# Kernel tuning notes

Hardware: AMD Instinct MI355X
Metric: run time of the kernel (lower is better)

Reference implementation:

```python
import jax, jax.numpy as jnp
import numpy as np
import math

N_HEAD = 32
HEAD_DIM = 64
ROTARY_DIM = 32
ROTARY_BASE = 10000.0
NEG_INF = -10000.0


def _rope_cos_sin(seqlen):
    # RotaryEmbedding._update_cos_sin_cache: inv_freq over even indices of rotary_dim
    inv_freq = 1.0 / (ROTARY_BASE ** (jnp.arange(0, ROTARY_DIM, 2, dtype=jnp.float32) / ROTARY_DIM))
    t = jnp.arange(seqlen, dtype=jnp.float32)
    freqs = jnp.outer(t, inv_freq)  # [s, rd/2]
    return jnp.cos(freqs), jnp.sin(freqs)


def _apply_rotary(t, cos, sin):
    # t: [b, s, h, d]; GPT-NeoX half-rotation on first ROTARY_DIM dims, pass-through rest
    half = ROTARY_DIM // 2
    x1 = t[..., :half]
    x2 = t[..., half:ROTARY_DIM]
    x_pass = t[..., ROTARY_DIM:]
    c = cos[:, None, :]  # [s, 1, rd/2] -> broadcasts over (b, s, h, rd/2)
    s_ = sin[:, None, :]
    return jnp.concatenate([x1 * c - x2 * s_, x1 * s_ + x2 * c, x_pass], axis=-1)


def setup_inputs() -> dict:
    key = jax.random.key(0)
    k1, k2, k3, k4, k5 = jax.random.split(key, 5)
    b, s, e = 2, 2048, 2048
    return {
        "x": jax.random.normal(k1, (b, s, e), dtype=jnp.float32),
        "Wqkv": jax.random.normal(k2, (e, 3 * e), dtype=jnp.float32) * 0.02,
        "bqkv": jax.random.normal(k3, (3 * e,), dtype=jnp.float32) * 0.02,
        "Wout": jax.random.normal(k4, (e, e), dtype=jnp.float32) * 0.02,
        "bout": jax.random.normal(k5, (e,), dtype=jnp.float32) * 0.02,
    }


def reference(x, Wqkv, bqkv, Wout, bout):
    b, s, e = x.shape
    # QKV projection -> [b, s, 3, h, d]
    qkv = (x @ Wqkv + bqkv).reshape(b, s, 3, N_HEAD, HEAD_DIM)
    cos, sin = _rope_cos_sin(s)
    q = _apply_rotary(qkv[:, :, 0], cos, sin)
    k = _apply_rotary(qkv[:, :, 1], cos, sin)
    v = qkv[:, :, 2]
    # Attention (SelfAttention/CrossAttention math, fp32, materialized scores)
    scale = 1.0 / math.sqrt(HEAD_DIM)
    scores = jnp.einsum('bthd,bshd->bhts', q, k * scale)  # [b, h, s, s]
    rows = jnp.arange(s)[:, None]
    cols = jnp.arange(s)[None, :]
    causal_mask = cols > rows  # seqlen_q == seqlen_k
    scores = jnp.where(causal_mask, NEG_INF, scores)
    attn = jax.nn.softmax(scores, axis=-1)
    out = jnp.einsum('bhts,bshd->bthd', attn, v).reshape(b, s, e)
    return out @ Wout + bout
```

## Files before the change

### kernel.cpp

```cpp
#include <hip/hip_runtime.h>


typedef _Float16 half8 __attribute__((ext_vector_type(8)));
typedef _Float16 half4 __attribute__((ext_vector_type(4)));
typedef float floatx4 __attribute__((ext_vector_type(4)));

#define GLD_LDS16(gp, sp)                                        \
  __builtin_amdgcn_global_load_lds(                              \
      (__attribute__((address_space(1))) void*)(gp),             \
      (__attribute__((address_space(3))) void*)(sp), 16, 0, 0)

__device__ __forceinline__ floatx4 mfma16(half8 a, half8 b, floatx4 c) {
  return __builtin_amdgcn_mfma_f32_16x16x32_f16(a, b, c, 0, 0, 0);
}
__device__ __forceinline__ floatx4 mfma16k16(half4 a, half4 b, floatx4 c) {
  return __builtin_amdgcn_mfma_f32_16x16x16f16(a, b, c, 0, 0, 0);
}

__global__ __launch_bounds__(256) void cvt_all_kernel(
    const float* __restrict__ x, _Float16* __restrict__ xh,
    const float* __restrict__ Wqkv, _Float16* __restrict__ wqkvt,
    const float* __restrict__ Wout, _Float16* __restrict__ woutt) {
  __shared__ float tile[64][65];
  int b = blockIdx.x, tid = threadIdx.x;
  if (b < 4096) {
    int idx = b * 256 + tid;
    const floatx4* p = (const floatx4*)x + (size_t)idx * 2;
    floatx4 a = p[0], b2 = p[1];
    half8 o;
#pragma unroll
    for (int j = 0; j < 4; ++j) { o[j] = (_Float16)a[j]; o[4 + j] = (_Float16)b2[j]; }
    *((half8*)xh + idx) = o;
    return;
  }
  const float* W;
  _Float16* Wt;
  int Kd, Nd, n0, k0;
  if (b < 7168) {
    int bb = b - 4096;
    W = Wqkv; Wt = wqkvt; Kd = 2048; Nd = 6144;
    n0 = (bb % 96) * 64; k0 = (bb / 96) * 64;
  } else {
    int bb = b - 7168;
    W = Wout; Wt = woutt; Kd = 2048; Nd = 2048;
    n0 = (bb % 32) * 64; k0 = (bb / 32) * 64;
  }
#pragma unroll
  for (int it = 0; it < 4; ++it) {
    int r = (tid >> 4) + it * 16;
    int c = (tid & 15) * 4;
    floatx4 v = *(const floatx4*)(W + (size_t)(k0 + r) * Nd + n0 + c);
    tile[r][c + 0] = v[0]; tile[r][c + 1] = v[1];
    tile[r][c + 2] = v[2]; tile[r][c + 3] = v[3];
  }
  __syncthreads();
#pragma unroll
  for (int it = 0; it < 2; ++it) {
    int r = (tid >> 3) + it * 32;
    int c = (tid & 7) * 8;
    half8 o;
#pragma unroll
    for (int j = 0; j < 8; ++j) o[j] = (_Float16)tile[c + j][r];
    *(half8*)(Wt + (size_t)(n0 + r) * Kd + k0 + c) = o;
  }
}

__global__ __launch_bounds__(512, 2) void gemm_qkv_kernel(
    const _Float16* __restrict__ A, const _Float16* __restrict__ Bt,
    const float* __restrict__ bias,
    _Float16* __restrict__ Qd, _Float16* __restrict__ Kkd,
    _Float16* __restrict__ Vd) {
  __shared__ __align__(16) _Float16 sA[2][16384];
  __shared__ __align__(16) _Float16 sB[2][12288];
  constexpr int KD = 2048;
  constexpr int NT = KD / 64;

  int tid = threadIdx.x, w = tid >> 6, l = tid & 63;
  int lr = l & 15, quad = l >> 4;
  int wr = w >> 1, wc = w & 1;
  int m0 = blockIdx.y * 256, n0 = blockIdx.x * 192;

  int csw0 = ((quad) ^ (lr & 7)) * 8;
  int csw1 = ((quad + 4) ^ (lr & 7)) * 8;

  const _Float16* pA[4];
  const _Float16* pB[3];
  {
    int rl = l >> 3;
    int cs = ((l & 7) ^ rl) * 8;
#pragma unroll
    for (int jj = 0; jj < 4; ++jj)
      pA[jj] = A + (size_t)(m0 + w * 32 + jj * 8 + rl) * KD + cs;
#pragma unroll
    for (int jj = 0; jj < 3; ++jj)
      pB[jj] = Bt + (size_t)(n0 + w * 24 + jj * 8 + rl) * KD + cs;
  }

#define STAGE_ALL(BUF, KT)                                                   \
  _Pragma("unroll") for (int jj = 0; jj < 4; ++jj)                           \
    GLD_LDS16(pA[jj] + (KT), &sA[BUF][(w * 32 + jj * 8) * 64]);              \
  _Pragma("unroll") for (int jj = 0; jj < 3; ++jj)                           \
    GLD_LDS16(pB[jj] + (KT), &sB[BUF][(w * 24 + jj * 8) * 64]);

  floatx4 z4 = {0.f, 0.f, 0.f, 0.f};
  floatx4 acc[4][6];
#pragma unroll
  for (int i = 0; i < 4; ++i)
#pragma unroll
    for (int j = 0; j < 6; ++j) acc[i][j] = z4;

  STAGE_ALL(0, 0);
  asm volatile("s_waitcnt vmcnt(0)" ::: "memory");
  __builtin_amdgcn_s_barrier();

  half8 af[4][2], bf[6][2];
#pragma unroll 2
  for (int t = 0; t < NT; ++t) {
    int buf = t & 1, nbuf = buf ^ 1;
    if (t + 1 < NT) { STAGE_ALL(nbuf, (t + 1) * 64); }
#pragma unroll
    for (int j = 0; j < 6; ++j) {
      int row_ = wc * 96 + j * 16 + lr;
      bf[j][0] = *(const half8*)&sB[buf][row_ * 64 + csw0];
      bf[j][1] = *(const half8*)&sB[buf][row_ * 64 + csw1];
    }
#pragma unroll
    for (int i = 0; i < 4; ++i) {
      int row_ = wr * 64 + i * 16 + lr;
      af[i][0] = *(const half8*)&sA[buf][row_ * 64 + csw0];
      af[i][1] = *(const half8*)&sA[buf][row_ * 64 + csw1];
    }
    __builtin_amdgcn_s_setprio(1);
#pragma unroll
    for (int j = 0; j < 6; ++j)
#pragma unroll
      for (int ks = 0; ks < 2; ++ks)
#pragma unroll
        for (int i = 0; i < 4; ++i)
          acc[i][j] = mfma16(af[i][ks], bf[j][ks], acc[i][j]);
    __builtin_amdgcn_s_setprio(0);
    asm volatile("s_waitcnt vmcnt(0)" ::: "memory");
    __builtin_amdgcn_s_barrier();
  }

  float bj[6];
#pragma unroll
  for (int j = 0; j < 6; ++j) bj[j] = bias[n0 + wc * 96 + j * 16 + lr];
  float freq = __expf(-(float)lr * 0.57564627324851148f);
#pragma unroll
  for (int j = 0; j < 6; ++j) {
    int cb = wc * 96 + j * 16;
    int cg = n0 + cb;
    int which = cg >> 11;
    int d0 = cb & 63;
    int hh = (cg & 2047) >> 6;
    if (which == 2) {
      int dd = d0 + lr;
#pragma unroll
      for (int i = 0; i < 4; ++i) {
        int m = m0 + wr * 64 + i * 16 + quad * 4;
        int bb = m >> 11, tt = m & 2047;
        half4 h;
#pragma unroll
        for (int r = 0; r < 4; ++r) h[r] = (_Float16)(acc[i][j][r] + bj[j]);
        *(half4*)&Vd[(((size_t)(bb * 32 + hh)) * 64 + dd) * 2048 + tt] = h;
      }
    } else if (d0 == 0) {
      _Float16* dst = which ? Kkd : Qd;
#pragma unroll
      for (int i = 0; i < 4; ++i)
#pragma unroll
        for (int r = 0; r < 4; ++r) {
          int m = m0 + wr * 64 + i * 16 + quad * 4 + r;
          int bb = m >> 11, tt = m & 2047;
          float sn, cs2;
          __sincosf((float)tt * freq, &sn, &cs2);
          float x1 = acc[i][j][r] + bj[j];
          float x2 = acc[i][j + 1][r] + bj[j + 1];
          _Float16* row = dst + ((size_t)(bb * 32 + hh) * 2048 + (size_t)tt) * 64;
          row[lr] = (_Float16)(x1 * cs2 - x2 * sn);
          row[lr + 16] = (_Float16)(x1 * sn + x2 * cs2);
        }
    } else if (d0 >= 32) {
      _Float16* dst = which ? Kkd : Qd;
#pragma unroll
      for (int i = 0; i < 4; ++i)
#pragma unroll
        for (int r = 0; r < 4; ++r) {
          int m = m0 + wr * 64 + i * 16 + quad * 4 + r;
          int bb = m >> 11, tt = m & 2047;
          _Float16* row = dst + ((size_t)(bb * 32 + hh) * 2048 + (size_t)tt) * 64;
          row[d0 + lr] = (_Float16)(acc[i][j][r] + bj[j]);
        }
    }
  }
#undef STAGE_ALL
}

__global__ __launch_bounds__(512, 2) void gemm_out_kernel(
    const _Float16* __restrict__ A, const _Float16* __restrict__ Bt,
    const float* __restrict__ bias, float* __restrict__ Co) {
  __shared__ __align__(16) _Float16 sA[2][16384];
  __shared__ __align__(16) _Float16 sB[2][8192];
  constexpr int KD = 2048;
  constexpr int NT = KD / 64;

  int tid = threadIdx.x, w = tid >> 6, l = tid & 63;
  int lr = l & 15, quad = l >> 4;
  int wr = w >> 1, wc = w & 1;
  int m0 = blockIdx.y * 256, n0 = blockIdx.x * 128;

  int csw0 = ((quad) ^ (lr & 7)) * 8;
  int csw1 = ((quad + 4) ^ (lr & 7)) * 8;

  const _Float16* pA[4];
  const _Float16* pB[2];
  {
    int rl = l >> 3;
    int cs = ((l & 7) ^ rl) * 8;
#pragma unroll
    for (int jj = 0; jj < 4; ++jj)
      pA[jj] = A + (size_t)(m0 + w * 32 + jj * 8 + rl) * KD + cs;
#pragma unroll
    for (int jj = 0; jj < 2; ++jj)
      pB[jj] = Bt + (size_t)(n0 + w * 16 + jj * 8 + rl) * KD + cs;
  }

#define STAGE_O(BUF, KT)                                                     \
  _Pragma("unroll") for (int jj = 0; jj < 4; ++jj)                           \
    GLD_LDS16(pA[jj] + (KT), &sA[BUF][(w * 32 + jj * 8) * 64]);              \
  _Pragma("unroll") for (int jj = 0; jj < 2; ++jj)                           \
    GLD_LDS16(pB[jj] + (KT), &sB[BUF][(w * 16 + jj * 8) * 64]);

  floatx4 z4 = {0.f, 0.f, 0.f, 0.f};
  floatx4 acc[4][4];
#pragma unroll
  for (int i = 0; i < 4; ++i)
#pragma unroll
    for (int j = 0; j < 4; ++j) acc[i][j] = z4;

  STAGE_O(0, 0);
  asm volatile("s_waitcnt vmcnt(0)" ::: "memory");
  __builtin_amdgcn_s_barrier();

  half8 af[4][2], bf[4][2];
#pragma unroll 2
  for (int t = 0; t < NT; ++t) {
    int buf = t & 1, nbuf = buf ^ 1;
    if (t + 1 < NT) { STAGE_O(nbuf, (t + 1) * 64); }
#pragma unroll
    for (int j = 0; j < 4; ++j) {
      int row_ = wc * 64 + j * 16 + lr;
      bf[j][0] = *(const half8*)&sB[buf][row_ * 64 + csw0];
      bf[j][1] = *(const half8*)&sB[buf][row_ * 64 + csw1];
    }
#pragma unroll
    for (int i = 0; i < 4; ++i) {
      int row_ = wr * 64 + i * 16 + lr;
      af[i][0] = *(const half8*)&sA[buf][row_ * 64 + csw0];
      af[i][1] = *(const half8*)&sA[buf][row_ * 64 + csw1];
    }
    __builtin_amdgcn_s_setprio(1);
#pragma unroll
    for (int j = 0; j < 4; ++j)
#pragma unroll
      for (int ks = 0; ks < 2; ++ks)
#pragma unroll
        for (int i = 0; i < 4; ++i)
          acc[i][j] = mfma16(af[i][ks], bf[j][ks], acc[i][j]);
    __builtin_amdgcn_s_setprio(0);
    asm volatile("s_waitcnt vmcnt(0)" ::: "memory");
    __builtin_amdgcn_s_barrier();
  }

#pragma unroll
  for (int j = 0; j < 4; ++j) {
    int n = n0 + wc * 64 + j * 16 + lr;
    float bj = bias[n];
#pragma unroll
    for (int i = 0; i < 4; ++i)
#pragma unroll
      for (int r = 0; r < 4; ++r) {
        int m = m0 + wr * 64 + i * 16 + quad * 4 + r;
        Co[(size_t)m * 2048 + n] = acc[i][j][r] + bj;
      }
  }
#undef STAGE_O
}

__global__ __launch_bounds__(256) void attn_kernel(
    const _Float16* __restrict__ Q, const _Float16* __restrict__ Kk,
    const _Float16* __restrict__ Vt, _Float16* __restrict__ O) {
  constexpr int S = 2048;
  int bh = blockIdx.x;
  int qt = 15 - blockIdx.y;
  int bb = bh >> 5, hh = bh & 31;
  const _Float16* Qb = Q + (size_t)bh * S * 64;
  const _Float16* Kb = Kk + (size_t)bh * S * 64;
  const _Float16* Vb = Vt + (size_t)bh * 64 * S;

  __shared__ __align__(16) _Float16 sK[128 * 72];
  __shared__ __align__(16) _Float16 sVt[64 * 136];

  int tid = threadIdx.x, w = tid >> 6, l = tid & 63;
  int lr = l & 15, quad = l >> 4;

  int rk = tid >> 3, ck = (tid & 7) * 8;
  int rv = tid >> 4, cv = (tid & 15) * 8;
  const _Float16* Kst = Kb + (size_t)rk * 64 + ck;
  const _Float16* Vst = Vb + (size_t)rv * S + cv;

  floatx4 z4 = {0.f, 0.f, 0.f, 0.f};
  int q0 = qt * 128;

  half8 qf[2][2];
#pragma unroll
  for (int qtl = 0; qtl < 2; ++qtl)
#pragma unroll
    for (int ks = 0; ks < 2; ++ks) {
      half8 v = *(const half8*)(Qb + (size_t)(q0 + w * 32 + qtl * 16 + lr) * 64 +
                                ks * 32 + quad * 8);
      qf[qtl][ks] = v * (_Float16)0.18033688f;
    }

  floatx4 Oa[4][2];
  float m_i[2] = {-1e30f, -1e30f}, l_i[2] = {0.f, 0.f};
#pragma unroll
  for (int dt = 0; dt < 4; ++dt)
#pragma unroll
    for (int qtl = 0; qtl < 2; ++qtl) Oa[dt][qtl] = z4;

  half8 kpre[4], vpre[4];
#pragma unroll
  for (int it = 0; it < 4; ++it) {
    kpre[it] = *(const half8*)(Kst + (size_t)it * 32 * 64);
    vpre[it] = *(const half8*)(Vst + (size_t)it * 16 * S);
  }

  for (int jt = 0; jt <= qt; ++jt) {
#pragma unroll
    for (int it = 0; it < 4; ++it) {
      *(half8*)&sK[(rk + it * 32) * 72 + ck] = kpre[it];
      *(half8*)&sVt[(rv + it * 16) * 136 + cv] = vpre[it];
    }
    if (jt < qt) {
      int kv1 = (jt + 1) * 128;
#pragma unroll
      for (int it = 0; it < 4; ++it) {
        kpre[it] = *(const half8*)(Kst + (size_t)(kv1 + it * 32) * 64);
        vpre[it] = *(const half8*)(Vst + kv1 + (size_t)it * 16 * S);
      }
    }
    __syncthreads();

    floatx4 Sa[2][8];
#pragma unroll
    for (int qtl = 0; qtl < 2; ++qtl)
#pragma unroll
      for (int kvt = 0; kvt < 8; ++kvt) Sa[qtl][kvt] = z4;
    __builtin_amdgcn_s_setprio(1);
#pragma unroll
    for (int ks = 0; ks < 2; ++ks) {
#pragma unroll
      for (int kvt = 0; kvt < 8; ++kvt) {
        half8 kf = *(const half8*)&sK[(kvt * 16 + lr) * 72 + ks * 32 + quad * 8];
        Sa[0][kvt] = mfma16(kf, qf[0][ks], Sa[0][kvt]);
        Sa[1][kvt] = mfma16(kf, qf[1][ks], Sa[1][kvt]);
      }
    }
    __builtin_amdgcn_s_setprio(0);

    if (jt == qt) {
#pragma unroll
      for (int qtl = 0; qtl < 2; ++qtl) {
        int q_loc = w * 32 + qtl * 16 + lr;
#pragma unroll
        for (int kvt = 0; kvt < 8; ++kvt) {
          int kv_base = kvt * 16 + quad * 4;
#pragma unroll
          for (int r = 0; r < 4; ++r)
            if (kv_base + r > q_loc) Sa[qtl][kvt][r] = -1e30f;
        }
      }
    }

#pragma unroll
    for (int qtl = 0; qtl < 2; ++qtl) {
      float mx = Sa[qtl][0][0];
#pragma unroll
      for (int kvt = 0; kvt < 8; ++kvt)
#pragma unroll
        for (int r = 0; r < 4; ++r) mx = fmaxf(mx, Sa[qtl][kvt][r]);
      mx = fmaxf(mx, __shfl_xor(mx, 16));
      mx = fmaxf(mx, __shfl_xor(mx, 32));
      float mnew = fmaxf(m_i[qtl], mx);
      if (!__all(mx <= m_i[qtl])) {
        float alpha = __builtin_amdgcn_exp2f(m_i[qtl] - mnew);
        l_i[qtl] *= alpha;
#pragma unroll
        for (int dt = 0; dt < 4; ++dt) Oa[dt][qtl] *= alpha;
      }
      m_i[qtl] = mnew;
      float rs = 0.f;
#pragma unroll
      for (int kvt = 0; kvt < 8; ++kvt)
#pragma unroll
        for (int r = 0; r < 4; ++r) {
          float p = __builtin_amdgcn_exp2f(Sa[qtl][kvt][r] - mnew);
          Sa[qtl][kvt][r] = p;
          rs += p;
        }
      rs += __shfl_xor(rs, 16);
      rs += __shfl_xor(rs, 32);
      l_i[qtl] += rs;
    }

    __builtin_amdgcn_s_setprio(1);
#pragma unroll
    for (int kvt = 0; kvt < 8; ++kvt) {
      half4 vf[4];
#pragma unroll
      for (int dt = 0; dt < 4; ++dt)
        vf[dt] = *(const half4*)&sVt[(dt * 16 + lr) * 136 + kvt * 16 + quad * 4];
      half4 pf[2];
#pragma unroll
      for (int qtl = 0; qtl < 2; ++qtl) {
        pf[qtl][0] = (_Float16)Sa[qtl][kvt][0];
        pf[qtl][1] = (_Float16)Sa[qtl][kvt][1];
        pf[qtl][2] = (_Float16)Sa[qtl][kvt][2];
        pf[qtl][3] = (_Float16)Sa[qtl][kvt][3];
      }
#pragma unroll
      for (int dt = 0; dt < 4; ++dt)
#pragma unroll
        for (int qtl = 0; qtl < 2; ++qtl)
          Oa[dt][qtl] = mfma16k16(vf[dt], pf[qtl], Oa[dt][qtl]);
    }
    __builtin_amdgcn_s_setprio(0);
    __syncthreads();
  }

  float inv0 = 1.0f / l_i[0], inv1 = 1.0f / l_i[1];
#pragma unroll
  for (int dt = 0; dt < 4; ++dt)
#pragma unroll
    for (int qtl = 0; qtl < 2; ++qtl) {
      float inv = qtl ? inv1 : inv0;
      floatx4 o = Oa[dt][qtl];
      half4 hv;
      hv[0] = (_Float16)(o[0] * inv); hv[1] = (_Float16)(o[1] * inv);
      hv[2] = (_Float16)(o[2] * inv); hv[3] = (_Float16)(o[3] * inv);
      *(half4*)&sK[(w * 32 + qtl * 16 + lr) * 72 + dt * 16 + quad * 4] = hv;
    }
  __syncthreads();
#pragma unroll
  for (int it = 0; it < 2; ++it) {
    int row = (tid >> 2) + it * 64;
    int t = q0 + row;
    _Float16* orow = O + ((size_t)(bb * 2048 + t)) * 2048 + hh * 64;
#pragma unroll
    for (int cc = 0; cc < 2; ++cc) {
      int col = (tid & 3) * 16 + cc * 8;
      *(half8*)(orow + col) = *(const half8*)&sK[row * 72 + col];
    }
  }
}

extern "C" void kernel_launch(void* const* d_in, const int* in_sizes, int n_in,
                              void* d_out, int out_size, void* d_ws, size_t ws_size,
                              hipStream_t stream) {
  (void)in_sizes; (void)n_in; (void)out_size; (void)ws_size;
  const float* x = (const float*)d_in[0];
  const float* Wqkv = (const float*)d_in[1];
  const float* bqkv = (const float*)d_in[2];
  const float* Wout = (const float*)d_in[3];
  const float* bout = (const float*)d_in[4];
  float* out = (float*)d_out;
  char* ws = (char*)d_ws;

  _Float16* xh    = (_Float16*)(ws + 0);
  _Float16* wqkvt = (_Float16*)(ws + 16777216);
  _Float16* Oh    = (_Float16*)(ws + 16777216);
  _Float16* Qh    = (_Float16*)(ws + 41943040);
  _Float16* Kh    = (_Float16*)(ws + 58720256);
  _Float16* Vth   = (_Float16*)(ws + 75497472);
  _Float16* woutt = (_Float16*)(ws + 92274688);

  cvt_all_kernel<<<8192, 256, 0, stream>>>(x, xh, Wqkv, wqkvt, Wout, woutt);
  gemm_qkv_kernel<<<dim3(32, 16), 512, 0, stream>>>(xh, wqkvt, bqkv, Qh, Kh, Vth);
  attn_kernel<<<dim3(64, 16), 256, 0, stream>>>(Qh, Kh, Vth, Oh);
  gemm_out_kernel<<<dim3(16, 16), 512, 0, stream>>>(Oh, woutt, bout, out);
}
```

Measured before the change: 390.8 us.

## Split conversion kernel, swizzle GEMM block order, drop conditional softmax rescale

```diff
diff --git a/kernel.cpp b/kernel.cpp
--- a/kernel.cpp
+++ b/kernel.cpp
@@ -17,34 +17,23 @@
   return __builtin_amdgcn_mfma_f32_16x16x16f16(a, b, c, 0, 0, 0);
 }
 
-__global__ __launch_bounds__(256) void cvt_all_kernel(
-    const float* __restrict__ x, _Float16* __restrict__ xh,
-    const float* __restrict__ Wqkv, _Float16* __restrict__ wqkvt,
-    const float* __restrict__ Wout, _Float16* __restrict__ woutt) {
+__global__ __launch_bounds__(256) void cvt_x_kernel(const float* __restrict__ x,
+                                                    _Float16* __restrict__ xh) {
+  int idx = blockIdx.x * 256 + threadIdx.x;
+  const floatx4* p = (const floatx4*)x + (size_t)idx * 2;
+  floatx4 a = p[0], b = p[1];
+  half8 o;
+#pragma unroll
+  for (int j = 0; j < 4; ++j) { o[j] = (_Float16)a[j]; o[4 + j] = (_Float16)b[j]; }
+  *((half8*)xh + idx) = o;
+}
+
+__global__ __launch_bounds__(256) void cvt_wt_kernel(const float* __restrict__ W,
+                                                     _Float16* __restrict__ Wt,
+                                                     int Kd, int Nd) {
   __shared__ float tile[64][65];
-  int b = blockIdx.x, tid = threadIdx.x;
-  if (b < 4096) {
-    int idx = b * 256 + tid;
-    const floatx4* p = (const floatx4*)x + (size_t)idx * 2;
-    floatx4 a = p[0], b2 = p[1];
-    half8 o;
-#pragma unroll
-    for (int j = 0; j < 4; ++j) { o[j] = (_Float16)a[j]; o[4 + j] = (_Float16)b2[j]; }
-    *((half8*)xh + idx) = o;
-    return;
-  }
-  const float* W;
-  _Float16* Wt;
-  int Kd, Nd, n0, k0;
-  if (b < 7168) {
-    int bb = b - 4096;
-    W = Wqkv; Wt = wqkvt; Kd = 2048; Nd = 6144;
-    n0 = (bb % 96) * 64; k0 = (bb / 96) * 64;
-  } else {
-    int bb = b - 7168;
-    W = Wout; Wt = woutt; Kd = 2048; Nd = 2048;
-    n0 = (bb % 32) * 64; k0 = (bb / 32) * 64;
-  }
+  int n0 = blockIdx.x * 64, k0 = blockIdx.y * 64;
+  int tid = threadIdx.x;
 #pragma unroll
   for (int it = 0; it < 4; ++it) {
     int r = (tid >> 4) + it * 16;
@@ -78,7 +67,10 @@
   int tid = threadIdx.x, w = tid >> 6, l = tid & 63;
   int lr = l & 15, quad = l >> 4;
   int wr = w >> 1, wc = w & 1;
-  int m0 = blockIdx.y * 256, n0 = blockIdx.x * 192;
+  int p = blockIdx.y * 32 + blockIdx.x;
+  int kx = p & 7, q = p >> 3;
+  int bx = kx + 8 * (q & 3), by = q >> 2;
+  int m0 = by * 256, n0 = bx * 192;
 
   int csw0 = ((quad) ^ (lr & 7)) * 8;
   int csw1 = ((quad + 4) ^ (lr & 7)) * 8;
@@ -208,7 +200,10 @@
   int tid = threadIdx.x, w = tid >> 6, l = tid & 63;
   int lr = l & 15, quad = l >> 4;
   int wr = w >> 1, wc = w & 1;
-  int m0 = blockIdx.y * 256, n0 = blockIdx.x * 128;
+  int p = blockIdx.y * 16 + blockIdx.x;
+  int kx = p & 7, q = p >> 3;
+  int bx = kx + 8 * (q & 1), by = q >> 1;
+  int m0 = by * 256, n0 = bx * 128;
 
   int csw0 = ((quad) ^ (lr & 7)) * 8;
   int csw1 = ((quad + 4) ^ (lr & 7)) * 8;
@@ -394,12 +389,7 @@
       mx = fmaxf(mx, __shfl_xor(mx, 16));
       mx = fmaxf(mx, __shfl_xor(mx, 32));
       float mnew = fmaxf(m_i[qtl], mx);
-      if (!__all(mx <= m_i[qtl])) {
-        float alpha = __builtin_amdgcn_exp2f(m_i[qtl] - mnew);
-        l_i[qtl] *= alpha;
-#pragma unroll
-        for (int dt = 0; dt < 4; ++dt) Oa[dt][qtl] *= alpha;
-      }
+      float alpha = __builtin_amdgcn_exp2f(m_i[qtl] - mnew);
       m_i[qtl] = mnew;
       float rs = 0.f;
 #pragma unroll
@@ -412,7 +402,9 @@
         }
       rs += __shfl_xor(rs, 16);
       rs += __shfl_xor(rs, 32);
-      l_i[qtl] += rs;
+      l_i[qtl] = l_i[qtl] * alpha + rs;
+#pragma unroll
+      for (int dt = 0; dt < 4; ++dt) Oa[dt][qtl] *= alpha;
     }
 
     __builtin_amdgcn_s_setprio(1);
@@ -486,7 +478,9 @@
   _Float16* Vth   = (_Float16*)(ws + 75497472);
   _Float16* woutt = (_Float16*)(ws + 92274688);
 
-  cvt_all_kernel<<<8192, 256, 0, stream>>>(x, xh, Wqkv, wqkvt, Wout, woutt);
+  cvt_x_kernel<<<4096, 256, 0, stream>>>(x, xh);
+  cvt_wt_kernel<<<dim3(96, 32), 256, 0, stream>>>(Wqkv, wqkvt, 2048, 6144);
+  cvt_wt_kernel<<<dim3(32, 32), 256, 0, stream>>>(Wout, woutt, 2048, 2048);
   gemm_qkv_kernel<<<dim3(32, 16), 512, 0, stream>>>(xh, wqkvt, bqkv, Qh, Kh, Vth);
   attn_kernel<<<dim3(64, 16), 256, 0, stream>>>(Qh, Kh, Vth, Oh);
   gemm_out_kernel<<<dim3(16, 16), 512, 0, stream>>>(Oh, woutt, bout, out);
```

Measured after the change: 387.1 us. No clear change (-0.9%).
